# Kernel tuning notes

Hardware: AMD Instinct MI355X
Metric: run time of the kernel (lower is better)

Reference implementation:

```python
import jax, jax.numpy as jnp
import numpy as np

EPS = 1e-5

def _sparse_conv(x, nbr, W):
    # x: [N, Cin], nbr: [N, K] indices into rows of x, W: [K, Cin, Cout]
    # Minkowski-style kernel-map conv: gather neighbor feats, contract per offset.
    return jnp.einsum('nkc,kcd->nd', x[nbr], W)

def _bn(x, gamma, beta):
    # BatchNorm over all points (training-mode, biased variance)
    mu = x.mean(axis=0)
    var = x.var(axis=0)
    return (x - mu) * jax.lax.rsqrt(var + EPS) * gamma + beta

def setup_inputs() -> dict:
    key = jax.random.key(0)
    ks = jax.random.split(key, 6)
    N, K, Cin, Cout = 100000, 27, 64, 128
    x = jax.random.normal(ks[0], (N, Cin), dtype=jnp.float32)
    nbr = jax.random.randint(ks[1], (N, K), 0, N, dtype=jnp.int64)
    W1 = jax.random.normal(ks[2], (K, Cin, Cout), dtype=jnp.float32) / np.sqrt(K * Cin)
    W2 = jax.random.normal(ks[3], (K, Cout, Cout), dtype=jnp.float32) / np.sqrt(K * Cout)
    Wd = jax.random.normal(ks[4], (Cin, Cout), dtype=jnp.float32) / np.sqrt(Cin)
    ones = jnp.ones((Cout,), jnp.float32)
    zeros = jnp.zeros((Cout,), jnp.float32)
    return {"x": x, "nbr": nbr, "W1": W1, "g1": ones, "b1": zeros,
            "W2": W2, "g2": ones, "b2": zeros, "Wd": Wd, "gd": ones, "bd": zeros}

def reference(x, nbr, W1, g1, b1, W2, g2, b2, Wd, gd, bd):
    h = jax.nn.relu(_bn(_sparse_conv(x, nbr, W1), g1, b1))
    h = jax.nn.relu(_bn(_sparse_conv(h, nbr, W2), g2, b2))
    # downsample branch (input_nc != output_nc): 1x1 sparse conv == matmul, + BN
    res = _bn(x @ Wd, gd, bd)
    return h + res
```

## Files before the change

### kernel.cpp

```cpp
#include <hip/hip_runtime.h>
#include <hip/hip_bf16.h>

typedef unsigned short u16;
typedef unsigned int   u32;

#define COUT 128
#define KNB  27

typedef __attribute__((ext_vector_type(8))) __bf16 bf16x8;
typedef __attribute__((ext_vector_type(4))) float  f32x4;

__device__ float g_sum[2][128], g_sq[2][128];
__device__ float g_colsum[64], g_G[4096];
__device__ float g_sc[3][128], g_sh[3][128];
__device__ int   g_f32;
__device__ int   g_i64;
__device__ __attribute__((aligned(16))) u16 g_W1t[KNB * 128 * 64];
__device__ __attribute__((aligned(16))) u16 g_W2t[KNB * 128 * 128];

__device__ __forceinline__ float b2f(u32 u) {
    union { float f; u32 i; } v; v.i = u << 16; return v.f;
}
__device__ __forceinline__ u16 f2b(float f) {
    union { float f; u32 i; } v; v.f = f;
    u32 r = v.i + 0x7fffu + ((v.i >> 16) & 1u);
    return (u16)(r >> 16);
}
__device__ __forceinline__ float ldf(const void* p, int i, bool f32) {
    return f32 ? ((const float*)p)[i] : b2f((u32)((const u16*)p)[i]);
}

__device__ __forceinline__ void gld16(const void* g, void* l) {
    __builtin_amdgcn_global_load_lds(
        (const __attribute__((address_space(1))) u32*)g,
        (__attribute__((address_space(3))) u32*)l, 16, 0, 0);
}

__device__ __forceinline__ void lds_sync() {
    asm volatile("s_waitcnt lgkmcnt(0)" ::: "memory");
    __builtin_amdgcn_s_barrier();
    asm volatile("" ::: "memory");
}

__global__ void probe_zero_kernel(const u16* __restrict__ g1w, const int* __restrict__ nbr)
{
    int t = threadIdx.x;
    if (t == 0) {
        g_f32 = (g1w[0] == 0) ? 1 : 0;
        g_i64 = ((nbr[1] | nbr[3] | nbr[5] | nbr[7]) == 0) ? 1 : 0;
    }
    for (int i = t; i < 128; i += 256) {
        g_sum[0][i] = 0.f; g_sq[0][i] = 0.f;
        g_sum[1][i] = 0.f; g_sq[1][i] = 0.f;
    }
    for (int i = t; i < 64; i += 256) g_colsum[i] = 0.f;
    for (int i = t; i < 4096; i += 256) g_G[i] = 0.f;
}

__global__ void convert_w_kernel(const void* __restrict__ W1, const void* __restrict__ W2,
                                 const void* __restrict__ x, u16* __restrict__ xb, int N)
{
    const bool f32 = (g_f32 != 0);
    const int total1 = KNB * 64 * 128;
    const int total2 = KNB * 128 * 128;
    const int stride = gridDim.x * 256;
    for (int e = blockIdx.x * 256 + threadIdx.x; e < total1 + total2; e += stride) {
        if (e < total1) {
            int k = e / (64 * 128), r = e % (64 * 128);
            int c = r / 128, d = r % 128;
            g_W1t[(k * 128 + d) * 64 + c] = f2b(ldf(W1, e, f32));
        } else {
            int e2 = e - total1;
            int k = e2 / (128 * 128), r = e2 % (128 * 128);
            int c = r / 128, d = r % 128;
            g_W2t[(k * 128 + d) * 128 + c] = f2b(ldf(W2, e2, f32));
        }
    }
    const int totalx4 = (N * 64) / 4;
    for (int e = blockIdx.x * 256 + threadIdx.x; e < totalx4; e += stride) {
        if (f32) {
            float4 v = ((const float4*)x)[e];
            ushort4 r;
            r.x = f2b(v.x); r.y = f2b(v.y); r.z = f2b(v.z); r.w = f2b(v.w);
            ((ushort4*)xb)[e] = r;
        } else {
            ((uint2*)xb)[e] = ((const uint2*)x)[e];
        }
    }
}

__global__ __launch_bounds__(256)
void bn_relu_kernel(u16* __restrict__ tmp, int N)
{
    const int t  = threadIdx.x;
    const int c0 = (t & 15) * 8;
    float sc[8], sh[8];
#pragma unroll
    for (int j = 0; j < 8; ++j) { sc[j] = g_sc[0][c0 + j]; sh[j] = g_sh[0][c0 + j]; }
    const int total = N * (COUT / 8);
    for (int e = blockIdx.x * 256 + t; e < total; e += gridDim.x * 256) {
        uint4 u = ((const uint4*)tmp)[e];
        float v[8] = { b2f(u.x & 0xffffu), b2f(u.x >> 16),
                       b2f(u.y & 0xffffu), b2f(u.y >> 16),
                       b2f(u.z & 0xffffu), b2f(u.z >> 16),
                       b2f(u.w & 0xffffu), b2f(u.w >> 16) };
#pragma unroll
        for (int j = 0; j < 8; ++j) v[j] = fmaxf(fmaf(v[j], sc[j], sh[j]), 0.f);
        uint4 o;
        o.x = (u32)f2b(v[0]) | ((u32)f2b(v[1]) << 16);
        o.y = (u32)f2b(v[2]) | ((u32)f2b(v[3]) << 16);
        o.z = (u32)f2b(v[4]) | ((u32)f2b(v[5]) << 16);
        o.w = (u32)f2b(v[6]) | ((u32)f2b(v[7]) << 16);
        ((uint4*)tmp)[e] = o;
    }
}

template<int CIN, bool OUTF32, int WSEL, int SSEL>
__global__ __launch_bounds__(256, 4)
void spconv_mfma(const u16* __restrict__ src, const int* __restrict__ nbr,
                 void* __restrict__ outv, int N)
{
    constexpr int CHUNKS = CIN / 32;
    constexpr int STEPS  = KNB * CHUNKS;
    const u16* __restrict__ Wt = (WSEL == 1) ? g_W1t : g_W2t;

    __shared__ __attribute__((aligned(16))) u16 As[2 * 4096];
    __shared__ __attribute__((aligned(16))) u16 Bs[2 * 4096];

    const int t    = threadIdx.x;
    const int lane = t & 63;
    const int w    = t >> 6;
    const int m    = lane & 15;
    const int q4   = lane >> 4;
    const int wm   = w >> 1;
    const int wn   = w & 1;
    const int n0   = blockIdx.x * 128;
    const int kst  = (g_i64 != 0) ? 2 : 1;

    u32 nb0[2];
#pragma unroll
    for (int i = 0; i < 2; ++i) {
        int gr  = n0 + (w + 4 * i) * 16 + m;
        int grc = (gr < N) ? gr : (N - 1);
        nb0[i] = (u32)grc * (u32)(KNB * kst);
    }

    f32x4 acc[4][4];
#pragma unroll
    for (int a = 0; a < 4; ++a)
#pragma unroll
        for (int b = 0; b < 4; ++b) acc[a][b] = (f32x4){0.f, 0.f, 0.f, 0.f};

    int idxE[2], idxO[2];

#define STEP_K(S)  ((S) / CHUNKS)
#define LOAD_IDX(DST, K) do { \
    int kk_ = (K) < KNB ? (K) : (KNB - 1); \
    DST[0] = nbr[nb0[0] + (u32)kk_ * (u32)kst]; \
    DST[1] = nbr[nb0[1] + (u32)kk_ * (u32)kst]; \
} while (0)

#define ISSUE_STEP(BUFO, IDX, K, S) do { \
    const int cb_ = ((S) & (CHUNKS - 1)) * 32; \
    _Pragma("unroll") \
    for (int i_ = 0; i_ < 2; ++i_) { \
        const int mt_ = w + 4 * i_; \
        u32 rw_ = (u32)(IDX)[i_]; if (rw_ >= (u32)N) rw_ = 0; \
        gld16(src + (size_t)rw_ * CIN + cb_ + q4 * 8, \
              &As[(BUFO) + mt_ * 512]); \
        gld16(Wt + ((size_t)(K) * 128 + mt_ * 16 + m) * CIN + cb_ + q4 * 8, \
              &Bs[(BUFO) + mt_ * 512]); \
    } \
} while (0)

#define MFMA_PHASE(LOFS) do { \
    __builtin_amdgcn_s_setprio(1); \
    bf16x8 afr_[4]; \
    _Pragma("unroll") \
    for (int mt_ = 0; mt_ < 4; ++mt_) \
        afr_[mt_] = *(const bf16x8*)&As[(LOFS) + (wm * 4 + mt_) * 512 + lane * 8]; \
    _Pragma("unroll") \
    for (int nt_ = 0; nt_ < 4; ++nt_) { \
        bf16x8 bfr_ = *(const bf16x8*)&Bs[(LOFS) + (wn * 4 + nt_) * 512 + lane * 8]; \
        _Pragma("unroll") \
        for (int mt_ = 0; mt_ < 4; ++mt_) \
            acc[mt_][nt_] = __builtin_amdgcn_mfma_f32_16x16x32_bf16( \
                afr_[mt_], bfr_, acc[mt_][nt_], 0, 0, 0); \
    } \
    __builtin_amdgcn_s_setprio(0); \
} while (0)

    LOAD_IDX(idxE, 0);
    LOAD_IDX(idxO, STEP_K(1));
    ISSUE_STEP(0, idxE, 0, 0);
    LOAD_IDX(idxE, STEP_K(2));

#pragma clang loop unroll(disable)
    for (int s = 0; s < STEPS; s += 2) {
        lds_sync();
        ISSUE_STEP(4096, idxO, STEP_K(s + 1), s + 1);
        LOAD_IDX(idxO, STEP_K(s + 3));
        asm volatile("s_waitcnt vmcnt(6)" ::: "memory");
        __builtin_amdgcn_s_barrier();
        asm volatile("" ::: "memory");
        MFMA_PHASE(0);

        lds_sync();
        if (s + 2 < STEPS) {
            ISSUE_STEP(0, idxE, STEP_K(s + 2), s + 2);
            LOAD_IDX(idxE, STEP_K(s + 4));
            asm volatile("s_waitcnt vmcnt(6)" ::: "memory");
        } else {
            asm volatile("s_waitcnt vmcnt(0)" ::: "memory");
        }
        __builtin_amdgcn_s_barrier();
        asm volatile("" ::: "memory");
        MFMA_PHASE(4096);
    }

    const int qq = lane >> 4, nn = lane & 15;
#pragma unroll
    for (int mt = 0; mt < 4; ++mt) {
#pragma unroll
        for (int r4 = 0; r4 < 4; ++r4) {
            int gr = n0 + (wm * 4 + mt) * 16 + qq * 4 + r4;
            if (gr < N) {
#pragma unroll
                for (int nt = 0; nt < 4; ++nt) {
                    float val = acc[mt][nt][r4];
                    size_t off = (size_t)gr * COUT + (wn * 4 + nt) * 16 + nn;
                    if constexpr (OUTF32) ((float*)outv)[off] = val;
                    else                  ((u16*)outv)[off]   = f2b(val);
                }
            }
        }
    }

    if constexpr (SSEL >= 0) {
        float sS[4], sQ[4];
#pragma unroll
        for (int nt = 0; nt < 4; ++nt) { sS[nt] = 0.f; sQ[nt] = 0.f; }
#pragma unroll
        for (int mt = 0; mt < 4; ++mt) {
#pragma unroll
            for (int r4 = 0; r4 < 4; ++r4) {
                int gr = n0 + (wm * 4 + mt) * 16 + qq * 4 + r4;
                bool ok = (gr < N);
#pragma unroll
                for (int nt = 0; nt < 4; ++nt) {
                    float v = ok ? acc[mt][nt][r4] : 0.f;
                    sS[nt] += v;
                    sQ[nt] = fmaf(v, v, sQ[nt]);
                }
            }
        }
#pragma unroll
        for (int nt = 0; nt < 4; ++nt) {
            sS[nt] += __shfl_xor(sS[nt], 16);
            sS[nt] += __shfl_xor(sS[nt], 32);
            sQ[nt] += __shfl_xor(sQ[nt], 16);
            sQ[nt] += __shfl_xor(sQ[nt], 32);
        }
        lds_sync();
        float* red = (float*)As;
        if (lane < 16) {
#pragma unroll
            for (int nt = 0; nt < 4; ++nt) {
                red[w * 64 + nt * 16 + lane]       = sS[nt];
                red[256 + w * 64 + nt * 16 + lane] = sQ[nt];
            }
        }
        lds_sync();
        if (t < 128) {
            int hi = t >> 6, lo = t & 63;
            float S = red[hi * 64 + lo] + red[(hi + 2) * 64 + lo];
            float Q = red[256 + hi * 64 + lo] + red[256 + (hi + 2) * 64 + lo];
            atomicAdd(&g_sum[SSEL][t], S);
            atomicAdd(&g_sq[SSEL][t],  Q);
        }
    }
#undef STEP_K
#undef LOAD_IDX
#undef ISSUE_STEP
#undef MFMA_PHASE
}

template<int SEL>
__global__ void finalize_kernel(const void* __restrict__ g, const void* __restrict__ b,
                                float invN)
{
    const bool f32 = (g_f32 != 0);
    int c = threadIdx.x;
    float mu  = g_sum[SEL][c] * invN;
    float var = fmaxf(g_sq[SEL][c] * invN - mu * mu, 0.f);
    float rs  = rsqrtf(var + 1e-5f);
    float sc  = rs * ldf(g, c, f32);
    g_sc[SEL][c] = sc;
    g_sh[SEL][c] = ldf(b, c, f32) - mu * sc;
}

__global__ __launch_bounds__(256)
void xstats_kernel(const void* __restrict__ xv, int N)
{
    __shared__ float xs[16 * 64];
    const bool f32 = (g_f32 != 0);
    const int t  = threadIdx.x;
    const int c  = t >> 2;
    const int cb = (t & 3) * 16;
    float acc[16];
#pragma unroll
    for (int j = 0; j < 16; ++j) acc[j] = 0.f;
    float cs = 0.f;

    for (int r0 = blockIdx.x * 16; r0 < N; r0 += gridDim.x * 16) {
        __syncthreads();
        {
            int e = t * 4;
            int rr = e >> 6, qq = e & 63;
            int row = r0 + rr;
            size_t off = (size_t)min(row, N - 1) * 64 + qq;
            bool ok = (row < N);
            float v0, v1, v2, v3;
            if (f32) {
                float4 vv = *(const float4*)((const float*)xv + off);
                v0 = vv.x; v1 = vv.y; v2 = vv.z; v3 = vv.w;
            } else {
                uint2 u = *(const uint2*)((const u16*)xv + off);
                v0 = b2f(u.x & 0xffffu); v1 = b2f(u.x >> 16);
                v2 = b2f(u.y & 0xffffu); v3 = b2f(u.y >> 16);
            }
            xs[e + 0] = ok ? v0 : 0.f;
            xs[e + 1] = ok ? v1 : 0.f;
            xs[e + 2] = ok ? v2 : 0.f;
            xs[e + 3] = ok ? v3 : 0.f;
        }
        __syncthreads();
#pragma unroll
        for (int rr = 0; rr < 16; ++rr) {
            float a = xs[rr * 64 + c];
#pragma unroll
            for (int j = 0; j < 16; ++j)
                acc[j] = fmaf(a, xs[rr * 64 + cb + j], acc[j]);
        }
        if (t < 64) {
#pragma unroll
            for (int rr = 0; rr < 16; ++rr) cs += xs[rr * 64 + t];
        }
    }
#pragma unroll
    for (int j = 0; j < 16; ++j) atomicAdd(&g_G[c * 64 + cb + j], acc[j]);
    if (t < 64) atomicAdd(&g_colsum[t], cs);
}

__global__ __launch_bounds__(128)
void finalize_d_kernel(const void* __restrict__ Wd, const void* __restrict__ gd,
                       const void* __restrict__ bd, float invN)
{
    __shared__ float Gs[64 * 64];
    const bool f32 = (g_f32 != 0);
    const int t = threadIdx.x;
    for (int e = t; e < 4096; e += 128) Gs[e] = g_G[e];
    __syncthreads();
    float w[64];
#pragma unroll
    for (int c = 0; c < 64; ++c) w[c] = ldf(Wd, c * 128 + t, f32);
    float s = 0.f, q = 0.f;
    for (int c = 0; c < 64; ++c) {
        float inner = 0.f;
#pragma unroll 8
        for (int cc = 0; cc < 64; ++cc) inner = fmaf(Gs[c * 64 + cc], w[cc], inner);
        q = fmaf(w[c], inner, q);
        s = fmaf(g_colsum[c], w[c], s);
    }
    float mu  = s * invN;
    float var = fmaxf(q * invN - mu * mu, 0.f);
    float rs  = rsqrtf(var + 1e-5f);
    float sc  = rs * ldf(gd, t, f32);
    g_sc[2][t] = sc;
    g_sh[2][t] = ldf(bd, t, f32) - mu * sc;
}

__global__ __launch_bounds__(256)
void finish_dense_kernel(const void* __restrict__ xv, const void* __restrict__ Wdv,
                         float* __restrict__ out, int N)
{
    __shared__ float Xs[64 * 68];
    __shared__ float Ws[64 * COUT];
    const bool f32 = (g_f32 != 0);
    const int t  = threadIdx.x;
    const int tx = t & 31;
    const int ty = t >> 5;
    const int n0 = blockIdx.x * 64;
    const int valid = min(64, N - n0);

    for (int e = t; e < 64 * 16; e += 256) {
        int mm = e >> 4;
        int qq = (e & 15) << 2;
        size_t off = (size_t)min(n0 + mm, N - 1) * 64 + qq;
        float v0, v1, v2, v3;
        if (f32) {
            float4 vv = *(const float4*)((const float*)xv + off);
            v0 = vv.x; v1 = vv.y; v2 = vv.z; v3 = vv.w;
        } else {
            uint2 u = *(const uint2*)((const u16*)xv + off);
            v0 = b2f(u.x & 0xffffu); v1 = b2f(u.x >> 16);
            v2 = b2f(u.y & 0xffffu); v3 = b2f(u.y >> 16);
        }
        *(float4*)&Xs[mm * 68 + qq] = make_float4(v0, v1, v2, v3);
    }
    if (f32) {
        const float* Wp = (const float*)Wdv;
        for (int e = t; e < (64 * COUT) / 8; e += 256) {
            int l = e << 3;
            float4 a = *(const float4*)(Wp + l);
            float4 b = *(const float4*)(Wp + l + 4);
            float* dst = &Ws[l];
            dst[0]=a.x; dst[1]=a.y; dst[2]=a.z; dst[3]=a.w;
            dst[4]=b.x; dst[5]=b.y; dst[6]=b.z; dst[7]=b.w;
        }
    } else {
        const u16* Wp = (const u16*)Wdv;
        for (int e = t; e < (64 * COUT) / 8; e += 256) {
            int l = e << 3;
            uint4 u = *(const uint4*)(Wp + l);
            float* dst = &Ws[l];
            dst[0] = b2f(u.x & 0xffffu); dst[1] = b2f(u.x >> 16);
            dst[2] = b2f(u.y & 0xffffu); dst[3] = b2f(u.y >> 16);
            dst[4] = b2f(u.z & 0xffffu); dst[5] = b2f(u.z >> 16);
            dst[6] = b2f(u.w & 0xffffu); dst[7] = b2f(u.w >> 16);
        }
    }
    __syncthreads();

    float acc[8][4];
#pragma unroll
    for (int mm = 0; mm < 8; ++mm)
#pragma unroll
        for (int j = 0; j < 4; ++j) acc[mm][j] = 0.f;

#pragma unroll 2
    for (int c = 0; c < 64; ++c) {
        float4 wv = *(const float4*)&Ws[c * COUT + tx * 4];
#pragma unroll
        for (int mm = 0; mm < 8; ++mm) {
            float a = Xs[(ty * 8 + mm) * 68 + c];
            acc[mm][0] = fmaf(a, wv.x, acc[mm][0]);
            acc[mm][1] = fmaf(a, wv.y, acc[mm][1]);
            acc[mm][2] = fmaf(a, wv.z, acc[mm][2]);
            acc[mm][3] = fmaf(a, wv.w, acc[mm][3]);
        }
    }

    const int d = tx * 4;
    float s2r[4] = {g_sc[1][d], g_sc[1][d+1], g_sc[1][d+2], g_sc[1][d+3]};
    float h2r[4] = {g_sh[1][d], g_sh[1][d+1], g_sh[1][d+2], g_sh[1][d+3]};
    float sdr[4] = {g_sc[2][d], g_sc[2][d+1], g_sc[2][d+2], g_sc[2][d+3]};
    float hdr[4] = {g_sh[2][d], g_sh[2][d+1], g_sh[2][d+2], g_sh[2][d+3]};
#pragma unroll
    for (int mm = 0; mm < 8; ++mm) {
        int rr = ty * 8 + mm;
        if (rr < valid) {
            float* p = out + (size_t)(n0 + rr) * COUT + d;
            float4 raw = *(float4*)p;
            float o0 = fmaxf(fmaf(raw.x, s2r[0], h2r[0]), 0.f) + fmaf(acc[mm][0], sdr[0], hdr[0]);
            float o1 = fmaxf(fmaf(raw.y, s2r[1], h2r[1]), 0.f) + fmaf(acc[mm][1], sdr[1], hdr[1]);
            float o2 = fmaxf(fmaf(raw.z, s2r[2], h2r[2]), 0.f) + fmaf(acc[mm][2], sdr[2], hdr[2]);
            float o3 = fmaxf(fmaf(raw.w, s2r[3], h2r[3]), 0.f) + fmaf(acc[mm][3], sdr[3], hdr[3]);
            *(float4*)p = make_float4(o0, o1, o2, o3);
        }
    }
}

extern "C" void kernel_launch(void* const* d_in, const int* in_sizes, int n_in,
                              void* d_out, int out_size, void* d_ws, size_t ws_size,
                              hipStream_t stream)
{
    const void* x   = d_in[0];
    const int*  nbr = (const int*)d_in[1];
    const void* W1  = d_in[2];
    const void* g1  = d_in[3];
    const void* b1  = d_in[4];
    const void* W2  = d_in[5];
    const void* g2  = d_in[6];
    const void* b2  = d_in[7];
    const void* Wd  = d_in[8];
    const void* gd  = d_in[9];
    const void* bd  = d_in[10];
    float* out = (float*)d_out;

    const int N = in_sizes[0] / 64;
    u16* tmp = (u16*)d_ws;
    u16* xb  = (u16*)d_out;

    const int nbm = (N + 127) / 128;
    const int nbf = (N + 63) / 64;
    const float invN = 1.f / (float)N;

    hipLaunchKernelGGL(probe_zero_kernel, dim3(1), dim3(256), 0, stream,
                       (const u16*)g1, nbr);
    hipLaunchKernelGGL(convert_w_kernel, dim3(1024), dim3(256), 0, stream,
                       W1, W2, x, xb, N);
    hipLaunchKernelGGL((spconv_mfma<64, false, 1, 0>), dim3(nbm), dim3(256), 0, stream,
                       xb, nbr, tmp, N);
    hipLaunchKernelGGL((finalize_kernel<0>), dim3(1), dim3(128), 0, stream, g1, b1, invN);
    hipLaunchKernelGGL(bn_relu_kernel, dim3(2048), dim3(256), 0, stream, tmp, N);
    hipLaunchKernelGGL((spconv_mfma<128, true, 2, 1>), dim3(nbm), dim3(256), 0, stream,
                       tmp, nbr, out, N);
    hipLaunchKernelGGL((finalize_kernel<1>), dim3(1), dim3(128), 0, stream, g2, b2, invN);
    hipLaunchKernelGGL(xstats_kernel, dim3(256), dim3(256), 0, stream, x, N);
    hipLaunchKernelGGL(finalize_d_kernel, dim3(1), dim3(128), 0, stream, Wd, gd, bd, invN);
    hipLaunchKernelGGL(finish_dense_kernel, dim3(nbf), dim3(256), 0, stream,
                       x, Wd, out, N);
}
```

Before: 827.7 us.

## Restructure sparse conv into 4-deep LDS ring with register-held weights and staged neighbor indices

The sparse conv kernel now uses 64-row tiles with 64-wide K chunks. Gathered activation rows go into a 4-stage swizzled LDS ring, while weight fragments load straight from global memory into registers and are double-buffered across steps. Neighbor indices for the whole tile are staged once in LDS rather than re-read from global memory every step. The aim is more loads in flight, no LDS traffic for weights, and no bank conflicts. In exchange it doubles the grid, reloads weights per block from L2, and adds register pressure.

After: 996.1 us. +20.3%, slower.

```diff
diff --git a/kernel.cpp b/kernel.cpp
--- a/kernel.cpp
+++ b/kernel.cpp
@@ -120,115 +120,154 @@
 void spconv_mfma(const u16* __restrict__ src, const int* __restrict__ nbr,
                  void* __restrict__ outv, int N)
 {
-    constexpr int CHUNKS = CIN / 32;
-    constexpr int STEPS  = KNB * CHUNKS;
+    constexpr int CHUNKS  = CIN / 64;
+    constexpr int STEPS   = KNB * CHUNKS;
+    constexpr int MAINEND = (STEPS & 1) ? (STEPS - 3) : (STEPS - 2);
     const u16* __restrict__ Wt = (WSEL == 1) ? g_W1t : g_W2t;
 
-    __shared__ __attribute__((aligned(16))) u16 As[2 * 4096];
-    __shared__ __attribute__((aligned(16))) u16 Bs[2 * 4096];
+    __shared__ __attribute__((aligned(16))) u16 ring[4 * 4096];
+    __shared__ u32 nbrl[64 * 28];
 
     const int t    = threadIdx.x;
     const int lane = t & 63;
     const int w    = t >> 6;
-    const int m    = lane & 15;
-    const int q4   = lane >> 4;
+    const int mh   = lane & 15;
+    const int qh   = lane >> 4;
     const int wm   = w >> 1;
     const int wn   = w & 1;
-    const int n0   = blockIdx.x * 128;
+    const int n0   = blockIdx.x * 64;
     const int kst  = (g_i64 != 0) ? 2 : 1;
 
-    u32 nb0[2];
-#pragma unroll
-    for (int i = 0; i < 2; ++i) {
-        int gr  = n0 + (w + 4 * i) * 16 + m;
+    const int rA   = w * 16 + (lane >> 3);
+    const int ga16 = ((lane & 7) ^ ((lane >> 3) & 7)) * 8;
+    const int lbB  = mh * CIN + qh * 8;
+    int axr[2];
+    axr[0] = ( qh      ^ (mh & 7)) * 8;
+    axr[1] = ((4 + qh) ^ (mh & 7)) * 8;
+
+    for (int e = t; e < 64 * KNB; e += 256) {
+        int row = e / KNB, kk = e - row * KNB;
+        int gr  = n0 + row;
         int grc = (gr < N) ? gr : (N - 1);
-        nb0[i] = (u32)grc * (u32)(KNB * kst);
-    }
-
-    f32x4 acc[4][4];
-#pragma unroll
-    for (int a = 0; a < 4; ++a)
+        nbrl[row * 28 + kk] = (u32)nbr[(size_t)grc * (KNB * kst) + (size_t)kk * kst];
+    }
+    __syncthreads();
+
+    f32x4 acc[2][4];
+#pragma unroll
+    for (int a = 0; a < 2; ++a)
 #pragma unroll
         for (int b = 0; b < 4; ++b) acc[a][b] = (f32x4){0.f, 0.f, 0.f, 0.f};
 
-    int idxE[2], idxO[2];
-
-#define STEP_K(S)  ((S) / CHUNKS)
-#define LOAD_IDX(DST, K) do { \
-    int kk_ = (K) < KNB ? (K) : (KNB - 1); \
-    DST[0] = nbr[nb0[0] + (u32)kk_ * (u32)kst]; \
-    DST[1] = nbr[nb0[1] + (u32)kk_ * (u32)kst]; \
+    uint4 bs0[8], bs1[8];
+    int ix0[2], ix1[2], ixE[2], ixO[2];
+
+#define KOF(S)  ((CHUNKS == 2) ? ((S) >> 1) : (S))
+#define CB(S)   ((CHUNKS == 2) ? (((S) & 1) * 64) : 0)
+
+#define IDXRD(DST, S) do { \
+    int kk_ = KOF(S); if (kk_ > KNB - 1) kk_ = KNB - 1; \
+    DST[0] = (int)nbrl[rA * 28 + kk_]; \
+    DST[1] = (int)nbrl[(rA + 8) * 28 + kk_]; \
 } while (0)
 
-#define ISSUE_STEP(BUFO, IDX, K, S) do { \
-    const int cb_ = ((S) & (CHUNKS - 1)) * 32; \
+#define ISSUE_A(S, IX) do { \
+    const int rb_ = ((S) & 3) * 4096; \
+    const int cb_ = CB(S); \
+    u32 r0_ = (u32)(IX)[0]; if (r0_ >= (u32)N) r0_ = 0; \
+    u32 r1_ = (u32)(IX)[1]; if (r1_ >= (u32)N) r1_ = 0; \
+    gld16(src + (size_t)r0_ * CIN + cb_ + ga16, &ring[rb_ + w * 1024]); \
+    gld16(src + (size_t)r1_ * CIN + cb_ + ga16, &ring[rb_ + w * 1024 + 512]); \
+} while (0)
+
+#define LOAD_B(BSET, S) do { \
+    const size_t kb_ = (size_t)KOF(S) * 128 * CIN + CB(S) + lbB; \
     _Pragma("unroll") \
-    for (int i_ = 0; i_ < 2; ++i_) { \
-        const int mt_ = w + 4 * i_; \
-        u32 rw_ = (u32)(IDX)[i_]; if (rw_ >= (u32)N) rw_ = 0; \
-        gld16(src + (size_t)rw_ * CIN + cb_ + q4 * 8, \
-              &As[(BUFO) + mt_ * 512]); \
-        gld16(Wt + ((size_t)(K) * 128 + mt_ * 16 + m) * CIN + cb_ + q4 * 8, \
-              &Bs[(BUFO) + mt_ * 512]); \
+    for (int nt_ = 0; nt_ < 4; ++nt_) { \
+        _Pragma("unroll") \
+        for (int ks_ = 0; ks_ < 2; ++ks_) \
+            BSET[nt_ * 2 + ks_] = *(const uint4*)(Wt + kb_ + \
+                (size_t)((wn * 4 + nt_) * 16) * CIN + ks_ * 32); \
     } \
 } while (0)
 
-#define MFMA_PHASE(LOFS) do { \
+#define MFMA_STEP(S, BSET) do { \
+    const int rb_ = ((S) & 3) * 4096; \
     __builtin_amdgcn_s_setprio(1); \
-    bf16x8 afr_[4]; \
     _Pragma("unroll") \
-    for (int mt_ = 0; mt_ < 4; ++mt_) \
-        afr_[mt_] = *(const bf16x8*)&As[(LOFS) + (wm * 4 + mt_) * 512 + lane * 8]; \
-    _Pragma("unroll") \
-    for (int nt_ = 0; nt_ < 4; ++nt_) { \
-        bf16x8 bfr_ = *(const bf16x8*)&Bs[(LOFS) + (wn * 4 + nt_) * 512 + lane * 8]; \
+    for (int ks_ = 0; ks_ < 2; ++ks_) { \
+        bf16x8 af_[2]; \
         _Pragma("unroll") \
-        for (int mt_ = 0; mt_ < 4; ++mt_) \
-            acc[mt_][nt_] = __builtin_amdgcn_mfma_f32_16x16x32_bf16( \
-                afr_[mt_], bfr_, acc[mt_][nt_], 0, 0, 0); \
+        for (int mt_ = 0; mt_ < 2; ++mt_) \
+            af_[mt_] = *(const bf16x8*)&ring[rb_ + (wm * 32 + mt_ * 16 + mh) * 64 + axr[ks_]]; \
+        _Pragma("unroll") \
+        for (int nt_ = 0; nt_ < 4; ++nt_) { \
+            bf16x8 bf_ = __builtin_bit_cast(bf16x8, BSET[nt_ * 2 + ks_]); \
+            _Pragma("unroll") \
+            for (int mt_ = 0; mt_ < 2; ++mt_) \
+                acc[mt_][nt_] = __builtin_amdgcn_mfma_f32_16x16x32_bf16( \
+                    af_[mt_], bf_, acc[mt_][nt_], 0, 0, 0); \
+        } \
     } \
     __builtin_amdgcn_s_setprio(0); \
 } while (0)
 
-    LOAD_IDX(idxE, 0);
-    LOAD_IDX(idxO, STEP_K(1));
-    ISSUE_STEP(0, idxE, 0, 0);
-    LOAD_IDX(idxE, STEP_K(2));
+#define WAITBAR(NSTR) do { \
+    asm volatile("s_waitcnt vmcnt(" NSTR ")" ::: "memory"); \
+    __builtin_amdgcn_s_barrier(); \
+    asm volatile("" ::: "memory"); \
+} while (0)
+
+    IDXRD(ix0, 0);
+    IDXRD(ix1, 1);
+    ISSUE_A(0, ix0);
+    ISSUE_A(1, ix1);
+    LOAD_B(bs0, 0);
+    IDXRD(ixE, 2);
+    IDXRD(ixO, 3);
 
 #pragma clang loop unroll(disable)
-    for (int s = 0; s < STEPS; s += 2) {
-        lds_sync();
-        ISSUE_STEP(4096, idxO, STEP_K(s + 1), s + 1);
-        LOAD_IDX(idxO, STEP_K(s + 3));
-        asm volatile("s_waitcnt vmcnt(6)" ::: "memory");
-        __builtin_amdgcn_s_barrier();
-        asm volatile("" ::: "memory");
-        MFMA_PHASE(0);
-
-        lds_sync();
-        if (s + 2 < STEPS) {
-            ISSUE_STEP(0, idxE, STEP_K(s + 2), s + 2);
-            LOAD_IDX(idxE, STEP_K(s + 4));
-            asm volatile("s_waitcnt vmcnt(6)" ::: "memory");
-        } else {
-            asm volatile("s_waitcnt vmcnt(0)" ::: "memory");
-        }
-        __builtin_amdgcn_s_barrier();
-        asm volatile("" ::: "memory");
-        MFMA_PHASE(4096);
-    }
-
-    const int qq = lane >> 4, nn = lane & 15;
-#pragma unroll
-    for (int mt = 0; mt < 4; ++mt) {
+    for (int s = 0; s < MAINEND; s += 2) {
+        LOAD_B(bs1, s + 1);
+        ISSUE_A(s + 2, ixE);
+        IDXRD(ixE, s + 4);
+        WAITBAR("20");
+        MFMA_STEP(s, bs0);
+        LOAD_B(bs0, s + 2);
+        ISSUE_A(s + 3, ixO);
+        IDXRD(ixO, s + 5);
+        WAITBAR("20");
+        MFMA_STEP(s + 1, bs1);
+    }
+
+    if constexpr (STEPS & 1) {
+        LOAD_B(bs1, MAINEND + 1);
+        ISSUE_A(MAINEND + 2, ixE);
+        WAITBAR("0");
+        MFMA_STEP(MAINEND, bs0);
+        LOAD_B(bs0, MAINEND + 2);
+        WAITBAR("0");
+        MFMA_STEP(MAINEND + 1, bs1);
+        WAITBAR("0");
+        MFMA_STEP(MAINEND + 2, bs0);
+    } else {
+        LOAD_B(bs1, MAINEND + 1);
+        WAITBAR("0");
+        MFMA_STEP(MAINEND, bs0);
+        WAITBAR("0");
+        MFMA_STEP(MAINEND + 1, bs1);
+    }
+
+#pragma unroll
+    for (int mt = 0; mt < 2; ++mt) {
 #pragma unroll
         for (int r4 = 0; r4 < 4; ++r4) {
-            int gr = n0 + (wm * 4 + mt) * 16 + qq * 4 + r4;
+            int gr = n0 + (wm * 2 + mt) * 16 + qh * 4 + r4;
             if (gr < N) {
 #pragma unroll
                 for (int nt = 0; nt < 4; ++nt) {
                     float val = acc[mt][nt][r4];
-                    size_t off = (size_t)gr * COUT + (wn * 4 + nt) * 16 + nn;
+                    size_t off = (size_t)gr * COUT + (wn * 4 + nt) * 16 + mh;
                     if constexpr (OUTF32) ((float*)outv)[off] = val;
                     else                  ((u16*)outv)[off]   = f2b(val);
                 }
@@ -241,10 +280,10 @@
 #pragma unroll
         for (int nt = 0; nt < 4; ++nt) { sS[nt] = 0.f; sQ[nt] = 0.f; }
 #pragma unroll
-        for (int mt = 0; mt < 4; ++mt) {
+        for (int mt = 0; mt < 2; ++mt) {
 #pragma unroll
             for (int r4 = 0; r4 < 4; ++r4) {
-                int gr = n0 + (wm * 4 + mt) * 16 + qq * 4 + r4;
+                int gr = n0 + (wm * 2 + mt) * 16 + qh * 4 + r4;
                 bool ok = (gr < N);
 #pragma unroll
                 for (int nt = 0; nt < 4; ++nt) {
@@ -262,7 +301,7 @@
             sQ[nt] += __shfl_xor(sQ[nt], 32);
         }
         lds_sync();
-        float* red = (float*)As;
+        float* red = (float*)ring;
         if (lane < 16) {
 #pragma unroll
             for (int nt = 0; nt < 4; ++nt) {
@@ -279,10 +318,13 @@
             atomicAdd(&g_sq[SSEL][t],  Q);
         }
     }
-#undef STEP_K
-#undef LOAD_IDX
-#undef ISSUE_STEP
-#undef MFMA_PHASE
+#undef KOF
+#undef CB
+#undef IDXRD
+#undef ISSUE_A
+#undef LOAD_B
+#undef MFMA_STEP
+#undef WAITBAR
 }
 
 template<int SEL>
@@ -492,7 +534,7 @@
     u16* tmp = (u16*)d_ws;
     u16* xb  = (u16*)d_out;
 
-    const int nbm = (N + 127) / 128;
+    const int nbm = (N + 63) / 64;
     const int nbf = (N + 63) / 64;
     const float invN = 1.f / (float)N;
 
```
